# Kernel optimization log

Measured on AMD Instinct MI355X. Metric: run time of the kernel, lower is better.

The kernel has to match this reference:

```python
import jax, jax.numpy as jnp
import numpy as np

N_EXC, N_INH = 4000, 1000
N = N_EXC + N_INH
DELAY = 15
TAU, DT = 20.0, 1.0
DECAY = 1.0 - DT / TAU  # 0.95 leaky-integration factor
V_TH, V_RESET = 1.0, 0.0
ALPHA = 4.0  # surrogate-gradient sharpness
CONN_P, J_W, G_INH = 0.1, 0.1, 5.0
T_STEPS, BATCH = 256, 8


@jax.custom_vjp
def spike_fn(x):
    return (x >= 0.0).astype(x.dtype)

def _spike_fwd(x):
    return spike_fn(x), x

def _spike_bwd(x, g):
    # sigmoid surrogate gradient: d/dx sigmoid(alpha*x)
    s = jax.nn.sigmoid(ALPHA * x)
    return (g * ALPHA * s * (1.0 - s),)

spike_fn.defvjp(_spike_fwd, _spike_bwd)


def setup_inputs() -> dict:
    key = jax.random.key(0)
    k1, k2 = jax.random.split(key, 2)
    # external drive (Poisson-like input current, positive mean)
    ext = jax.random.normal(k1, (T_STEPS, BATCH, N), dtype=jnp.float32) * 0.5 + 0.2
    # Brunel connectivity: prob CONN_P, exc cols weight +J, inh cols weight -g*J
    mask = (jax.random.uniform(k2, (N, N)) < CONN_P).astype(jnp.float32)
    col_w = jnp.concatenate([jnp.full((N_EXC,), J_W, jnp.float32),
                             jnp.full((N_INH,), -G_INH * J_W, jnp.float32)])
    W = mask * col_w[None, :]  # W[i, j] = weight from presyn j to postsyn i
    return {"external_input": ext, "W": W}


def reference(external_input, W):
    T, B, n = external_input.shape

    def step(carry, x_t):
        buf, v, idx = carry
        delayed = jax.lax.dynamic_index_in_dim(buf, idx, axis=0, keepdims=False)  # [B, N]
        i_total = delayed @ W.T + x_t                 # recurrent + external current
        v_new = v * DECAY + i_total                   # leaky integration
        s = spike_fn(v_new - V_TH)                    # threshold crossing
        v_out = (1.0 - s) * v_new + s * V_RESET       # hard reset
        buf = jax.lax.dynamic_update_index_in_dim(buf, s, idx, axis=0)
        return (buf, v_out, (idx + 1) % DELAY), (s, v_out)

    buf0 = jnp.zeros((DELAY, B, n), external_input.dtype)
    v0 = jnp.zeros((B, n), external_input.dtype)
    _, (spikes, vs) = jax.lax.scan(step, (buf0, v0, jnp.int32(0)), external_input)
    return spikes, vs
```

## Files before the change

### kernel.cpp

```cpp
#include <hip/hip_runtime.h>
#include <stdint.h>

#define NN      5000
#define NB      8
#define TSTEPS  256
#define NDELAY  15
#define NW      157
#define NIPAD   5120
#define RW      160
#define IPB     256
#define BPB     20
#define NBLK    (NB*BPB)
#define CH      4
#define NCHUNK  (TSTEPS/CH)
#define BARSTRIDE 16
#define RING_DEPTH 256

#define MASK_BYTES (NW*NIPAD*4)
#define BAR_OFF    MASK_BYTES
#define BAR_BYTES  (64*BARSTRIDE*4)
#define RING_OFF   (BAR_OFF + BAR_BYTES)
#define RING_BYTES (RING_DEPTH*NB*RW*4)
#define ZERO_BYTES (RING_OFF + RING_BYTES)

__global__ void _Brunel_build_mask(const float* __restrict__ W,
                                   uint32_t* __restrict__ maskT2)
{
    int j = blockIdx.x * blockDim.x + threadIdx.x;
    int i = blockIdx.y;
    int lane = threadIdx.x & 63;
    bool nz = false;
    if (j < NN) nz = (W[(size_t)i * NN + j] != 0.0f);
    unsigned long long m = __ballot(nz);
    if ((lane & 31) == 0 && j < NN) {
        uint32_t wd = (lane == 0) ? (uint32_t)m : (uint32_t)(m >> 32);
        maskT2[(size_t)(j >> 5) * NIPAD + i] = wd;
    }
}

__global__ void __launch_bounds__(IPB, 1) _Brunel_persist(
    const float* __restrict__ ext,
    const uint32_t* __restrict__ maskT2,
    uint32_t* __restrict__ ring,
    int* __restrict__ barc,
    float* __restrict__ out_spk,
    float* __restrict__ out_vs)
{
    const int tx   = threadIdx.x;
    const int bb   = blockIdx.x;
    const int b    = bb / BPB;
    const int i    = (bb % BPB) * IPB + tx;
    const bool act = (i < NN);
    const int lane = tx & 63;

    __shared__ __align__(16) uint32_t s_mask[IPB][156];
    __shared__ uint32_t s_mask156[IPB];

    for (int w = 0; w < NW; ++w) {
        uint32_t mv = maskT2[(size_t)w * NIPAD + i];
        if (w < 156) s_mask[tx][w] = mv; else s_mask156[tx] = mv;
    }
    __syncthreads();

    float v = 0.0f;

    for (int t0 = 0, m = 0; t0 < TSTEPS; t0 += CH, ++m) {
        float x0 = 0.f, x1 = 0.f, x2 = 0.f, x3 = 0.f;
        if (act) {
            const float* e0 = ext + ((size_t)t0 * NB + b) * NN + i;
            const size_t st = (size_t)NB * NN;
            x0 = e0[0]; x1 = e0[st]; x2 = e0[2 * st]; x3 = e0[3 * st];
        }

        if (m >= 3) {
            if (tx == 0) {
                const int* c3 = barc + (size_t)(m - 3) * BARSTRIDE;
                while (__hip_atomic_load(c3, __ATOMIC_RELAXED,
                                         __HIP_MEMORY_SCOPE_AGENT) < NBLK)
                    __builtin_amdgcn_s_sleep(2);
            }
            __syncthreads();
        }

        const uint4* __restrict__ s0 =
            (const uint4*)(ring + ((size_t)(t0 + 0) * NB + b) * RW);
        const uint4* __restrict__ s1 =
            (const uint4*)(ring + ((size_t)(t0 + 1) * NB + b) * RW);
        const uint4* __restrict__ s2 =
            (const uint4*)(ring + ((size_t)(t0 + 2) * NB + b) * RW);
        const uint4* __restrict__ s3 =
            (const uint4*)(ring + ((size_t)(t0 + 3) * NB + b) * RW);

        int cE0 = 0, cE1 = 0, cE2 = 0, cE3 = 0;
        int cI0 = 0, cI1 = 0, cI2 = 0, cI3 = 0;
        const uint32_t* __restrict__ mrow = s_mask[tx];

#pragma unroll 4
        for (int c = 0; c < 31; ++c) {
            uint4 m4 = *(const uint4*)(mrow + 4 * c);
            uint4 a0 = s0[c], a1 = s1[c], a2 = s2[c], a3 = s3[c];
            cE0 += __popc(m4.x & a0.x) + __popc(m4.y & a0.y)
                 + __popc(m4.z & a0.z) + __popc(m4.w & a0.w);
            cE1 += __popc(m4.x & a1.x) + __popc(m4.y & a1.y)
                 + __popc(m4.z & a1.z) + __popc(m4.w & a1.w);
            cE2 += __popc(m4.x & a2.x) + __popc(m4.y & a2.y)
                 + __popc(m4.z & a2.z) + __popc(m4.w & a2.w);
            cE3 += __popc(m4.x & a3.x) + __popc(m4.y & a3.y)
                 + __popc(m4.z & a3.z) + __popc(m4.w & a3.w);
        }
        {
            uint4 m4 = *(const uint4*)(mrow + 124);
            uint4 a0 = s0[31], a1 = s1[31], a2 = s2[31], a3 = s3[31];
            cE0 += __popc(m4.x & a0.x);
            cI0 += __popc(m4.y & a0.y) + __popc(m4.z & a0.z) + __popc(m4.w & a0.w);
            cE1 += __popc(m4.x & a1.x);
            cI1 += __popc(m4.y & a1.y) + __popc(m4.z & a1.z) + __popc(m4.w & a1.w);
            cE2 += __popc(m4.x & a2.x);
            cI2 += __popc(m4.y & a2.y) + __popc(m4.z & a2.z) + __popc(m4.w & a2.w);
            cE3 += __popc(m4.x & a3.x);
            cI3 += __popc(m4.y & a3.y) + __popc(m4.z & a3.z) + __popc(m4.w & a3.w);
        }
#pragma unroll 4
        for (int c = 32; c < 39; ++c) {
            uint4 m4 = *(const uint4*)(mrow + 4 * c);
            uint4 a0 = s0[c], a1 = s1[c], a2 = s2[c], a3 = s3[c];
            cI0 += __popc(m4.x & a0.x) + __popc(m4.y & a0.y)
                 + __popc(m4.z & a0.z) + __popc(m4.w & a0.w);
            cI1 += __popc(m4.x & a1.x) + __popc(m4.y & a1.y)
                 + __popc(m4.z & a1.z) + __popc(m4.w & a1.w);
            cI2 += __popc(m4.x & a2.x) + __popc(m4.y & a2.y)
                 + __popc(m4.z & a2.z) + __popc(m4.w & a2.w);
            cI3 += __popc(m4.x & a3.x) + __popc(m4.y & a3.y)
                 + __popc(m4.z & a3.z) + __popc(m4.w & a3.w);
        }
        {
            uint32_t mL = s_mask156[tx];
            cI0 += __popc(mL & ((const uint32_t*)s0)[156]);
            cI1 += __popc(mL & ((const uint32_t*)s1)[156]);
            cI2 += __popc(mL & ((const uint32_t*)s2)[156]);
            cI3 += __popc(mL & ((const uint32_t*)s3)[156]);
        }

#define BRUNEL_STEP(kk, xk)                                                   \
        {                                                                     \
            const int t = t0 + kk;                                            \
            float cur = 0.1f * (float)cE##kk - 0.5f * (float)cI##kk;          \
            v = v * 0.95f + (cur + xk);                                       \
            bool s = act && (v >= 1.0f);                                      \
            float sflag = s ? 1.0f : 0.0f;                                    \
            float vout  = s ? 0.0f : v;                                       \
            if (act) {                                                        \
                size_t o = ((size_t)t * NB + b) * NN + i;                     \
                out_spk[o] = sflag;                                           \
                out_vs[o]  = vout;                                            \
            }                                                                 \
            v = vout;                                                         \
            unsigned long long bm = __ballot(s);                              \
            if ((lane & 31) == 0 && act && t <= TSTEPS - 1 - NDELAY) {        \
                uint32_t wd = (lane == 0) ? (uint32_t)bm : (uint32_t)(bm >> 32); \
                __hip_atomic_store(                                           \
                    &ring[((size_t)(t + NDELAY) * NB + b) * RW + (i >> 5)],   \
                    wd, __ATOMIC_RELAXED, __HIP_MEMORY_SCOPE_AGENT);          \
            }                                                                 \
        }
        BRUNEL_STEP(0, x0)
        BRUNEL_STEP(1, x1)
        BRUNEL_STEP(2, x2)
        BRUNEL_STEP(3, x3)
#undef BRUNEL_STEP

        asm volatile("s_waitcnt vmcnt(0)" ::: "memory");
        __syncthreads();
        if (tx == 0)
            __hip_atomic_fetch_add(barc + (size_t)m * BARSTRIDE, 1,
                                   __ATOMIC_RELAXED, __HIP_MEMORY_SCOPE_AGENT);
    }
}

extern "C" void kernel_launch(void* const* d_in, const int* in_sizes, int n_in,
                              void* d_out, int out_size, void* d_ws, size_t ws_size,
                              hipStream_t stream)
{
    const float* ext = (const float*)d_in[0];
    const float* W   = (const float*)d_in[1];

    float* out_spk = (float*)d_out;
    float* out_vs  = out_spk + (size_t)TSTEPS * NB * NN;

    uint8_t*  ws   = (uint8_t*)d_ws;
    uint32_t* mask = (uint32_t*)(ws);
    int*      barc = (int*)(ws + BAR_OFF);
    uint32_t* ring = (uint32_t*)(ws + RING_OFF);

    hipMemsetAsync(ws, 0, ZERO_BYTES, stream);

    dim3 gmask(NIPAD / IPB, NN);
    _Brunel_build_mask<<<gmask, IPB, 0, stream>>>(W, mask);

    _Brunel_persist<<<NBLK, IPB, 0, stream>>>(ext, mask, ring, barc,
                                              out_spk, out_vs);
}
```

Measured before the change: 542.5 us.

## Split each neuron's popcount reduction across two half-wave lanes

Each block now has 512 threads, and each neuron's presynaptic word range is split between the two 32-lane halves of a wave. Each half accumulates excitatory and inhibitory counts packed into one 32-bit word (low and high 16 bits). The halves are combined with a cross-half shuffle. Only the lower half writes outputs and a single lane stores the spike ballot word. This halves the serial popcount chain per thread, which sits on the per-step critical path of the persistent recurrent loop. In exchange it adds shuffle traffic and doubles threads per block while keeping the same block count.

Measured after the change: 659.6 us. +21.6%, slower.

```diff
diff --git a/kernel.cpp b/kernel.cpp
--- a/kernel.cpp
+++ b/kernel.cpp
@@ -8,15 +8,15 @@
 #define NW      157
 #define NIPAD   5120
 #define RW      160
-#define IPB     256
-#define BPB     20
-#define NBLK    (NB*BPB)
+#define IPB     512
+#define NSL     20
+#define NBLK    (NB*NSL)
 #define CH      4
 #define NCHUNK  (TSTEPS/CH)
 #define BARSTRIDE 16
 #define RING_DEPTH 256
 
-#define MASK_BYTES (NW*NIPAD*4)
+#define MASK_BYTES (160*NIPAD*4)
 #define BAR_OFF    MASK_BYTES
 #define BAR_BYTES  (64*BARSTRIDE*4)
 #define RING_OFF   (BAR_OFF + BAR_BYTES)
@@ -38,7 +38,7 @@
     }
 }
 
-__global__ void __launch_bounds__(IPB, 1) _Brunel_persist(
+__global__ void __launch_bounds__(IPB, 2) _Brunel_persist(
     const float* __restrict__ ext,
     const uint32_t* __restrict__ maskT2,
     uint32_t* __restrict__ ring,
@@ -47,22 +47,36 @@
     float* __restrict__ out_vs)
 {
     const int tx   = threadIdx.x;
+    const int wv   = tx >> 6;
+    const int lane = tx & 63;
+    const int h    = lane >> 5;
+    const int ln32 = lane & 31;
+    const int nl   = wv * 32 + ln32;
     const int bb   = blockIdx.x;
-    const int b    = bb / BPB;
-    const int i    = (bb % BPB) * IPB + tx;
+    const int b    = bb / NSL;
+    const int sl   = bb % NSL;
+    const int i    = sl * 256 + nl;
     const bool act = (i < NN);
-    const int lane = tx & 63;
-
-    __shared__ __align__(16) uint32_t s_mask[IPB][156];
-    __shared__ uint32_t s_mask156[IPB];
-
-    for (int w = 0; w < NW; ++w) {
-        uint32_t mv = maskT2[(size_t)w * NIPAD + i];
-        if (w < 156) s_mask[tx][w] = mv; else s_mask156[tx] = mv;
+
+    __shared__ __align__(16) uint32_t s_mask[256][156];
+    __shared__ uint32_t s_mask156[256];
+
+    for (int w2 = 0; w2 < 79; ++w2) {
+        int w = 78 * h + w2;
+        if (w < NW) {
+            uint32_t mv = maskT2[(size_t)w * NIPAD + i];
+            if (w < 156) s_mask[nl][w] = mv; else s_mask156[nl] = mv;
+        }
     }
     __syncthreads();
 
     float v = 0.0f;
+
+    const int      qoff  = h ? 19 : 0;
+    const uint32_t shA   = h ? 16u : 0u;
+    const uint32_t kill  = h ? 0xFFFFFFFFu : 0u;
+    const uint32_t sel156= h ? 0xFFFFFFFFu : 0u;
+    const uint32_t* __restrict__ mrow = s_mask[nl];
 
     for (int t0 = 0, m = 0; t0 < TSTEPS; t0 += CH, ++m) {
         float x0 = 0.f, x1 = 0.f, x2 = 0.f, x3 = 0.f;
@@ -91,82 +105,72 @@
         const uint4* __restrict__ s3 =
             (const uint4*)(ring + ((size_t)(t0 + 3) * NB + b) * RW);
 
-        int cE0 = 0, cE1 = 0, cE2 = 0, cE3 = 0;
-        int cI0 = 0, cI1 = 0, cI2 = 0, cI3 = 0;
-        const uint32_t* __restrict__ mrow = s_mask[tx];
+        uint32_t acc0 = 0, acc1 = 0, acc2 = 0, acc3 = 0;
+
+#define HALF_WORD(c, j, MW, A0, A1, A2, A3)                                   \
+        if (4 * (c) + (j) < 49) {                 \
+            acc0 += (uint32_t)__popc((MW) & (A0));                            \
+            acc1 += (uint32_t)__popc((MW) & (A1));                            \
+            acc2 += (uint32_t)__popc((MW) & (A2));                            \
+            acc3 += (uint32_t)__popc((MW) & (A3));                            \
+        } else {                             \
+            acc0 += (uint32_t)__popc((MW) & (A0)) << shA;                     \
+            acc1 += (uint32_t)__popc((MW) & (A1)) << shA;                     \
+            acc2 += (uint32_t)__popc((MW) & (A2)) << shA;                     \
+            acc3 += (uint32_t)__popc((MW) & (A3)) << shA;                     \
+        }
 
 #pragma unroll 4
-        for (int c = 0; c < 31; ++c) {
-            uint4 m4 = *(const uint4*)(mrow + 4 * c);
-            uint4 a0 = s0[c], a1 = s1[c], a2 = s2[c], a3 = s3[c];
-            cE0 += __popc(m4.x & a0.x) + __popc(m4.y & a0.y)
-                 + __popc(m4.z & a0.z) + __popc(m4.w & a0.w);
-            cE1 += __popc(m4.x & a1.x) + __popc(m4.y & a1.y)
-                 + __popc(m4.z & a1.z) + __popc(m4.w & a1.w);
-            cE2 += __popc(m4.x & a2.x) + __popc(m4.y & a2.y)
-                 + __popc(m4.z & a2.z) + __popc(m4.w & a2.w);
-            cE3 += __popc(m4.x & a3.x) + __popc(m4.y & a3.y)
-                 + __popc(m4.z & a3.z) + __popc(m4.w & a3.w);
-        }
+        for (int c = 0; c < 20; ++c) {
+            uint4 m4 = *(const uint4*)(mrow + 4 * (qoff + c));
+            if (c == 19) { m4.x &= kill; m4.y &= kill; m4.z &= kill; m4.w &= kill; }
+            uint4 a0 = s0[qoff + c], a1 = s1[qoff + c],
+                  a2 = s2[qoff + c], a3 = s3[qoff + c];
+            HALF_WORD(c, 0, m4.x, a0.x, a1.x, a2.x, a3.x)
+            HALF_WORD(c, 1, m4.y, a0.y, a1.y, a2.y, a3.y)
+            HALF_WORD(c, 2, m4.z, a0.z, a1.z, a2.z, a3.z)
+            HALF_WORD(c, 3, m4.w, a0.w, a1.w, a2.w, a3.w)
+        }
+#undef HALF_WORD
         {
-            uint4 m4 = *(const uint4*)(mrow + 124);
-            uint4 a0 = s0[31], a1 = s1[31], a2 = s2[31], a3 = s3[31];
-            cE0 += __popc(m4.x & a0.x);
-            cI0 += __popc(m4.y & a0.y) + __popc(m4.z & a0.z) + __popc(m4.w & a0.w);
-            cE1 += __popc(m4.x & a1.x);
-            cI1 += __popc(m4.y & a1.y) + __popc(m4.z & a1.z) + __popc(m4.w & a1.w);
-            cE2 += __popc(m4.x & a2.x);
-            cI2 += __popc(m4.y & a2.y) + __popc(m4.z & a2.z) + __popc(m4.w & a2.w);
-            cE3 += __popc(m4.x & a3.x);
-            cI3 += __popc(m4.y & a3.y) + __popc(m4.z & a3.z) + __popc(m4.w & a3.w);
-        }
-#pragma unroll 4
-        for (int c = 32; c < 39; ++c) {
-            uint4 m4 = *(const uint4*)(mrow + 4 * c);
-            uint4 a0 = s0[c], a1 = s1[c], a2 = s2[c], a3 = s3[c];
-            cI0 += __popc(m4.x & a0.x) + __popc(m4.y & a0.y)
-                 + __popc(m4.z & a0.z) + __popc(m4.w & a0.w);
-            cI1 += __popc(m4.x & a1.x) + __popc(m4.y & a1.y)
-                 + __popc(m4.z & a1.z) + __popc(m4.w & a1.w);
-            cI2 += __popc(m4.x & a2.x) + __popc(m4.y & a2.y)
-                 + __popc(m4.z & a2.z) + __popc(m4.w & a2.w);
-            cI3 += __popc(m4.x & a3.x) + __popc(m4.y & a3.y)
-                 + __popc(m4.z & a3.z) + __popc(m4.w & a3.w);
-        }
-        {
-            uint32_t mL = s_mask156[tx];
-            cI0 += __popc(mL & ((const uint32_t*)s0)[156]);
-            cI1 += __popc(mL & ((const uint32_t*)s1)[156]);
-            cI2 += __popc(mL & ((const uint32_t*)s2)[156]);
-            cI3 += __popc(mL & ((const uint32_t*)s3)[156]);
-        }
-
-#define BRUNEL_STEP(kk, xk)                                                   \
+            uint32_t mL = s_mask156[nl] & sel156;
+            acc0 += (uint32_t)__popc(mL & ((const uint32_t*)s0)[156]) << 16;
+            acc1 += (uint32_t)__popc(mL & ((const uint32_t*)s1)[156]) << 16;
+            acc2 += (uint32_t)__popc(mL & ((const uint32_t*)s2)[156]) << 16;
+            acc3 += (uint32_t)__popc(mL & ((const uint32_t*)s3)[156]) << 16;
+        }
+
+        acc0 += (uint32_t)__shfl_xor((int)acc0, 32);
+        acc1 += (uint32_t)__shfl_xor((int)acc1, 32);
+        acc2 += (uint32_t)__shfl_xor((int)acc2, 32);
+        acc3 += (uint32_t)__shfl_xor((int)acc3, 32);
+
+#define BRUNEL_STEP(kk, ACC, xk)                                              \
         {                                                                     \
             const int t = t0 + kk;                                            \
-            float cur = 0.1f * (float)cE##kk - 0.5f * (float)cI##kk;          \
+            int cE = (int)((ACC) & 0xFFFFu);                                  \
+            int cI = (int)((ACC) >> 16);                                      \
+            float cur = 0.1f * (float)cE - 0.5f * (float)cI;                  \
             v = v * 0.95f + (cur + xk);                                       \
             bool s = act && (v >= 1.0f);                                      \
-            float sflag = s ? 1.0f : 0.0f;                                    \
-            float vout  = s ? 0.0f : v;                                       \
-            if (act) {                                                        \
+            float vout = s ? 0.0f : v;                                        \
+            if (act && h == 0) {                                              \
                 size_t o = ((size_t)t * NB + b) * NN + i;                     \
-                out_spk[o] = sflag;                                           \
+                out_spk[o] = s ? 1.0f : 0.0f;                                 \
                 out_vs[o]  = vout;                                            \
             }                                                                 \
             v = vout;                                                         \
             unsigned long long bm = __ballot(s);                              \
-            if ((lane & 31) == 0 && act && t <= TSTEPS - 1 - NDELAY) {        \
-                uint32_t wd = (lane == 0) ? (uint32_t)bm : (uint32_t)(bm >> 32); \
+            if (lane == 0 && t <= TSTEPS - 1 - NDELAY) {                      \
                 __hip_atomic_store(                                           \
-                    &ring[((size_t)(t + NDELAY) * NB + b) * RW + (i >> 5)],   \
-                    wd, __ATOMIC_RELAXED, __HIP_MEMORY_SCOPE_AGENT);          \
+                    &ring[((size_t)(t + NDELAY) * NB + b) * RW + sl * 8 + wv],\
+                    (uint32_t)bm, __ATOMIC_RELAXED, __HIP_MEMORY_SCOPE_AGENT);\
             }                                                                 \
         }
-        BRUNEL_STEP(0, x0)
-        BRUNEL_STEP(1, x1)
-        BRUNEL_STEP(2, x2)
-        BRUNEL_STEP(3, x3)
+        BRUNEL_STEP(0, acc0, x0)
+        BRUNEL_STEP(1, acc1, x1)
+        BRUNEL_STEP(2, acc2, x2)
+        BRUNEL_STEP(3, acc3, x3)
 #undef BRUNEL_STEP
 
         asm volatile("s_waitcnt vmcnt(0)" ::: "memory");
@@ -194,8 +198,8 @@
 
     hipMemsetAsync(ws, 0, ZERO_BYTES, stream);
 
-    dim3 gmask(NIPAD / IPB, NN);
-    _Brunel_build_mask<<<gmask, IPB, 0, stream>>>(W, mask);
+    dim3 gmask(NIPAD / 256, NN);
+    _Brunel_build_mask<<<gmask, 256, 0, stream>>>(W, mask);
 
     _Brunel_persist<<<NBLK, IPB, 0, stream>>>(ext, mask, ring, barc,
                                               out_spk, out_vs);
```
